# Kernel tuning notes

Hardware: AMD Instinct MI355X
Metric: run time of the kernel (lower is better)

The kernel has to match this reference:

```python
import jax, jax.numpy as jnp
import numpy as np

N_NODES = 100000
N_EDGES = 1600000
N_GRAPHS = 64
IN_DIM = 128
HID = 64
N_CLASSES = 10


def setup_inputs() -> dict:
    key = jax.random.key(0)
    ks = jax.random.split(key, 8)
    x = jax.random.normal(ks[0], (N_NODES, IN_DIM), jnp.float32)
    edge_index = jax.random.randint(ks[1], (2, N_EDGES), 0, N_NODES, jnp.int32)
    graph_id = jnp.sort(jax.random.randint(ks[2], (N_NODES,), 0, N_GRAPHS, jnp.int32))
    W1 = jax.random.normal(ks[3], (IN_DIM, HID), jnp.float32) / np.sqrt(IN_DIM)
    b1 = jnp.zeros((HID,), jnp.float32)
    W2 = jax.random.normal(ks[4], (HID, HID), jnp.float32) / np.sqrt(HID)
    b2 = jnp.zeros((HID,), jnp.float32)
    attn_W = jax.random.normal(ks[5], (HID, 1), jnp.float32) / np.sqrt(HID)
    attn_b = jnp.zeros((1,), jnp.float32)
    cls_W = jax.random.normal(ks[6], (HID, N_CLASSES), jnp.float32) / np.sqrt(HID)
    cls_b = jnp.zeros((N_CLASSES,), jnp.float32)
    return {"x": x, "edge_index": edge_index, "graph_id": graph_id,
            "W1": W1, "b1": b1, "W2": W2, "b2": b2,
            "attn_W": attn_W, "attn_b": attn_b, "cls_W": cls_W, "cls_b": cls_b}


def _graph_conv(h, W, b, src, dst, norm_out, norm_in):
    # DGL GraphConv, norm='both': D_in^{-1/2} A D_out^{-1/2} (h W) + b
    h = h @ W                                  # [N, out]
    h = h * norm_out[:, None]                  # scale by src out-degree^{-1/2}
    m = jax.ops.segment_sum(h[src], dst, num_segments=N_NODES)  # SpMM aggregation
    return m * norm_in[:, None] + b


def reference(x, edge_index, graph_id, W1, b1, W2, b2, attn_W, attn_b, cls_W, cls_b):
    src, dst = edge_index[0], edge_index[1]
    ones_e = jnp.ones((src.shape[0],), jnp.float32)
    deg_out = jnp.clip(jax.ops.segment_sum(ones_e, src, num_segments=N_NODES), 1.0)
    deg_in = jnp.clip(jax.ops.segment_sum(ones_e, dst, num_segments=N_NODES), 1.0)
    norm_out = jax.lax.rsqrt(deg_out)
    norm_in = jax.lax.rsqrt(deg_in)

    h = jax.nn.relu(_graph_conv(x, W1, b1, src, dst, norm_out, norm_in))
    h = jax.nn.relu(_graph_conv(h, W2, b2, src, dst, norm_out, norm_in))

    hw = jax.nn.sigmoid(h @ attn_W + attn_b)   # [N, 1] attention gate
    h = h * hw

    # mean_nodes: per-graph mean pooling
    sums = jax.ops.segment_sum(h, graph_id, num_segments=N_GRAPHS)        # [G, HID]
    cnts = jnp.clip(jax.ops.segment_sum(jnp.ones((N_NODES,), jnp.float32), graph_id,
                                        num_segments=N_GRAPHS), 1.0)
    hg = sums / cnts[:, None]
    out = hg @ cls_W + cls_b                   # [G, n_classes]
    return out, hw
```

## Files before the change

kernel.cpp:

```cpp
#include <hip/hip_runtime.h>
#include <stdint.h>


#define N_NODES   100000
#define N_EDGES   1600000
#define N_GRAPHS  64
#define IN_DIM    128
#define HID       64
#define N_CLASSES 10

#define NBUCK     391
#define P1B       196
#define EPB       8192
#define GB_BLOCKS 391
#define MTILES    6250
#define GEMM_BLOCKS 1563
#define SPMM_BLOCKS 3125
#define POOL_SLICES 32
#define WS_NEED   33885952u

typedef __attribute__((ext_vector_type(8))) short short8v;
typedef __attribute__((ext_vector_type(4))) float f32x4;
typedef __bf16 bf16x8 __attribute__((ext_vector_type(8)));

__device__ __forceinline__ f32x4 mfma16(short8v a, short8v b, f32x4 c) {
  return __builtin_amdgcn_mfma_f32_16x16x32_bf16(
      __builtin_bit_cast(bf16x8, a), __builtin_bit_cast(bf16x8, b), c, 0, 0, 0);
}

__device__ __forceinline__ float bf2f(unsigned short u) {
  unsigned int v = ((unsigned int)u) << 16;
  float f;
  __builtin_memcpy(&f, &v, 4);
  return f;
}

__device__ __forceinline__ unsigned short f2bf(float f) {
  unsigned int x;
  __builtin_memcpy(&x, &f, 4);
  unsigned int lsb = (x >> 16) & 1u;
  x += 0x7fffu + lsb;
  return (unsigned short)(x >> 16);
}

__device__ __forceinline__ void unpack_bf2(unsigned int u, float& lo, float& hi) {
  unsigned int a = u << 16;
  unsigned int b = u & 0xffff0000u;
  __builtin_memcpy(&lo, &a, 4);
  __builtin_memcpy(&hi, &b, 4);
}

__device__ __forceinline__ float ldf(const void* p, int i, int mode) {
  return mode ? bf2f(((const unsigned short*)p)[i]) : ((const float*)p)[i];
}

__global__ __launch_bounds__(256) void fallback_kernel(unsigned short* __restrict__ out,
                                                       int n) {
  int i = blockIdx.x * 256 + threadIdx.x;
  if (i < n) out[i] = 0;
}

__global__ __launch_bounds__(256) void wcvt_kernel(
    const unsigned short* __restrict__ xu,
    const void* __restrict__ W1, const void* __restrict__ W2,
    const void* __restrict__ b1, const void* __restrict__ b2,
    const void* __restrict__ attnW, const void* __restrict__ attnb,
    const void* __restrict__ clsW, const void* __restrict__ clsb,
    unsigned short* __restrict__ W1hf, unsigned short* __restrict__ W1lf,
    unsigned short* __restrict__ W2hf, unsigned short* __restrict__ W2lf,
    float* __restrict__ b1f, float* __restrict__ b2f,
    float* __restrict__ attnWf, float* __restrict__ attnbf,
    float* __restrict__ clsWf, float* __restrict__ clsbf,
    int* __restrict__ flag) {
  __shared__ int cnt[4];
  __shared__ int smode;
  int tid = (int)threadIdx.x;
  unsigned u = xu[2 * tid];
  int e = (int)((u >> 7) & 0xFF);
  int ok = (e >= 110 && e <= 132) ? 1 : 0;
  unsigned long long m = __ballot(ok);
  if ((tid & 63) == 0) cnt[tid >> 6] = __popcll(m);
  __syncthreads();
  if (tid == 0) {
    smode = (cnt[0] + cnt[1] + cnt[2] + cnt[3] > 128) ? 1 : 0;
    if (blockIdx.x == 0) {
      flag[0] = smode;
      flag[1] = 1;
    }
  }
  __syncthreads();
  int mode = smode;

  int i = blockIdx.x * 256 + tid;
  if (i < 1024) {
    int tile = i >> 6, lane = i & 63;
    int kt = tile >> 2, ct = tile & 3;
#pragma unroll
    for (int j = 0; j < 8; ++j) {
      int k = kt * 32 + ((lane >> 4) << 3) + j;
      int d = (ct << 4) + (lane & 15);
      float v = ldf(W1, k * HID + d, mode);
      unsigned short h = f2bf(v);
      unsigned short l = f2bf(v - bf2f(h));
      W1hf[i * 8 + j] = h;
      W1lf[i * 8 + j] = l;
    }
  } else if (i < 1536) {
    int ii = i - 1024;
    int tile = ii >> 6, lane = ii & 63;
    int kt = tile >> 2, ct = tile & 3;
#pragma unroll
    for (int j = 0; j < 8; ++j) {
      int k = kt * 32 + ((lane >> 4) << 3) + j;
      int d = (ct << 4) + (lane & 15);
      float v = ldf(W2, k * HID + d, mode);
      unsigned short h = f2bf(v);
      unsigned short l = f2bf(v - bf2f(h));
      W2hf[ii * 8 + j] = h;
      W2lf[ii * 8 + j] = l;
    }
  }
  if (i < HID) {
    b1f[i] = ldf(b1, i, mode);
    b2f[i] = ldf(b2, i, mode);
    attnWf[i] = ldf(attnW, i, mode);
  }
  if (i == 0) attnbf[0] = ldf(attnb, 0, mode);
  if (i < HID * N_CLASSES) clsWf[i] = ldf(clsW, i, mode);
  if (i < N_CLASSES) clsbf[i] = ldf(clsb, i, mode);
}

template <int K, bool SCALE>
__device__ __forceinline__ void gemm_tile(
    const void* __restrict__ A, const unsigned short* __restrict__ Whf,
    const unsigned short* __restrict__ Wlf, const float* __restrict__ norm_out,
    unsigned short* __restrict__ out, int mode, int mtile, int lane) {
  int n0 = mtile << 4;
  int row = lane & 15;
  int kg = lane >> 4;
  f32x4 acc0 = {0.f, 0.f, 0.f, 0.f};
  f32x4 acc1 = {0.f, 0.f, 0.f, 0.f};
  f32x4 acc2 = {0.f, 0.f, 0.f, 0.f};
  f32x4 acc3 = {0.f, 0.f, 0.f, 0.f};
  const short8v* whb0 = (const short8v*)Whf + lane;
  const short8v* wlb0 = (const short8v*)Wlf + lane;
  if (mode) {
    const unsigned short* xr = (const unsigned short*)A + (size_t)(n0 + row) * K + (kg << 3);
#pragma unroll
    for (int kt = 0; kt < K / 32; ++kt) {
      uint4 va = *(const uint4*)(xr + kt * 32);
      short8v xh = __builtin_bit_cast(short8v, va);
      const short8v* wh = whb0 + (size_t)(kt * 4) * 64;
      const short8v* wl = wlb0 + (size_t)(kt * 4) * 64;
      acc0 = mfma16(xh, wh[0], acc0);
      acc1 = mfma16(xh, wh[64], acc1);
      acc2 = mfma16(xh, wh[128], acc2);
      acc3 = mfma16(xh, wh[192], acc3);
      acc0 = mfma16(xh, wl[0], acc0);
      acc1 = mfma16(xh, wl[64], acc1);
      acc2 = mfma16(xh, wl[128], acc2);
      acc3 = mfma16(xh, wl[192], acc3);
    }
  } else {
    const float* xr = (const float*)A + (size_t)(n0 + row) * K + (kg << 3);
#pragma unroll
    for (int kt = 0; kt < K / 32; ++kt) {
      float4 a0 = *(const float4*)(xr + kt * 32);
      float4 a1 = *(const float4*)(xr + kt * 32 + 4);
      float xv[8] = {a0.x, a0.y, a0.z, a0.w, a1.x, a1.y, a1.z, a1.w};
      short8v xh, xl;
#pragma unroll
      for (int j = 0; j < 8; ++j) {
        unsigned short h = f2bf(xv[j]);
        unsigned short l = f2bf(xv[j] - bf2f(h));
        xh[j] = (short)h;
        xl[j] = (short)l;
      }
      const short8v* wh = whb0 + (size_t)(kt * 4) * 64;
      const short8v* wl = wlb0 + (size_t)(kt * 4) * 64;
      acc0 = mfma16(xh, wh[0], acc0);
      acc1 = mfma16(xh, wh[64], acc1);
      acc2 = mfma16(xh, wh[128], acc2);
      acc3 = mfma16(xh, wh[192], acc3);
      acc0 = mfma16(xh, wl[0], acc0);
      acc1 = mfma16(xh, wl[64], acc1);
      acc2 = mfma16(xh, wl[128], acc2);
      acc3 = mfma16(xh, wl[192], acc3);
      acc0 = mfma16(xl, wh[0], acc0);
      acc1 = mfma16(xl, wh[64], acc1);
      acc2 = mfma16(xl, wh[128], acc2);
      acc3 = mfma16(xl, wh[192], acc3);
    }
  }
  int col = lane & 15;
#pragma unroll
  for (int i = 0; i < 4; ++i) {
    int n = n0 + (kg << 2) + i;
    float s = SCALE ? norm_out[n] : 1.f;
    size_t rb = (size_t)n << 6;
    out[rb + col]      = f2bf(acc0[i] * s);
    out[rb + 16 + col] = f2bf(acc1[i] * s);
    out[rb + 32 + col] = f2bf(acc2[i] * s);
    out[rb + 48 + col] = f2bf(acc3[i] * s);
  }
}

__global__ __launch_bounds__(256) void fatA_kernel(
    const int* __restrict__ ei, int* __restrict__ blkhistD,
    int* __restrict__ blkhistS,
    const int* __restrict__ gid, int* __restrict__ gstart,
    const void* __restrict__ x, const unsigned short* __restrict__ W1hf,
    const unsigned short* __restrict__ W1lf, unsigned short* __restrict__ bufA,
    const int* __restrict__ flag) {
  int b = (int)blockIdx.x;
  int t = (int)threadIdx.x;
  if (b < P1B) {
    __shared__ int hD[NBUCK];
    __shared__ int hS[NBUCK];
    for (int i = t; i < NBUCK; i += 256) { hD[i] = 0; hS[i] = 0; }
    __syncthreads();
    int base_e = b * EPB;
    for (int s = 0; s < EPB / 1024; ++s) {
      int e4 = base_e + s * 1024 + t * 4;
      if (e4 < N_EDGES) {
        int4 s4 = *(const int4*)(ei + e4);
        int4 d4 = *(const int4*)(ei + N_EDGES + e4);
        int ss[4] = {s4.x, s4.y, s4.z, s4.w};
        int dd[4] = {d4.x, d4.y, d4.z, d4.w};
#pragma unroll
        for (int j = 0; j < 4; ++j) {
          if ((unsigned)ss[j] < N_NODES) atomicAdd(&hS[ss[j] >> 8], 1);
          if ((unsigned)dd[j] < N_NODES) atomicAdd(&hD[dd[j] >> 8], 1);
        }
      }
    }
    __syncthreads();
    for (int i = t; i < NBUCK; i += 256) {
      blkhistD[b * NBUCK + i] = hD[i];
      blkhistS[b * NBUCK + i] = hS[i];
    }
  } else if (b < P1B + GEMM_BLOCKS) {
    int mode = flag[0];
    int mtile = (b - P1B) * 4 + (t >> 6);
    if (mtile < MTILES)
      gemm_tile<IN_DIM, false>(x, W1hf, W1lf, (const float*)0, bufA, mode,
                               mtile, t & 63);
  } else {
    int bb = b - P1B - GEMM_BLOCKS;
    int n = bb * 256 + t;
    if (n >= N_NODES) return;
    int gc = gid[n] & (N_GRAPHS - 1);
    if (n == 0) {
      for (int g = 0; g <= gc; ++g) gstart[g] = 0;
    } else {
      int gp = gid[n - 1] & (N_GRAPHS - 1);
      for (int g = gp + 1; g <= gc; ++g) gstart[g] = n;
    }
    if (n == N_NODES - 1) {
      for (int g = gc + 1; g <= N_GRAPHS; ++g) gstart[g] = N_NODES;
    }
  }
}

__global__ __launch_bounds__(512) void bucket_scan_kernel(
    int* __restrict__ blkhistD, int* __restrict__ blkhistS,
    int* __restrict__ bstart_d, int* __restrict__ bstart_s) {
  int* hist = (blockIdx.x == 0) ? blkhistD : blkhistS;
  int* bst  = (blockIdx.x == 0) ? bstart_d : bstart_s;
  int u = (int)threadIdx.x;
  int tot = 0;
  if (u < NBUCK) {
    for (int blk = 0; blk < P1B; ++blk) tot += hist[blk * NBUCK + u];
  }
  __shared__ int smA[512];
  __shared__ int smB[512];
  smA[u] = tot;
  __syncthreads();
  int* a = smA;
  int* bq = smB;
  for (int off = 1; off < 512; off <<= 1) {
    int v = a[u];
    if (u >= off) v += a[u - off];
    bq[u] = v;
    __syncthreads();
    int* tmp = a; a = bq; bq = tmp;
  }
  int excl = a[u] - tot;
  if (u <= NBUCK) bst[u] = excl;
  if (u < NBUCK) {
    int off2 = excl;
    for (int blk = 0; blk < P1B; ++blk) {
      int h = hist[blk * NBUCK + u];
      hist[blk * NBUCK + u] = off2;
      off2 += h;
    }
  }
}

__global__ __launch_bounds__(256) void part_scatter_kernel(
    const int* __restrict__ ei, const int* __restrict__ blkbaseD,
    const int* __restrict__ blkbaseS,
    unsigned int* __restrict__ edstP, int* __restrict__ esrc) {
  __shared__ int cD[NBUCK];
  __shared__ int cS[NBUCK];
  int b = (int)blockIdx.x;
  int t = (int)threadIdx.x;
  for (int i = t; i < NBUCK; i += 256) {
    cD[i] = blkbaseD[b * NBUCK + i];
    cS[i] = blkbaseS[b * NBUCK + i];
  }
  __syncthreads();
  int base_e = b * EPB;
  for (int s = 0; s < EPB / 1024; ++s) {
    int e4 = base_e + s * 1024 + t * 4;
    if (e4 < N_EDGES) {
      int4 s4 = *(const int4*)(ei + e4);
      int4 d4 = *(const int4*)(ei + N_EDGES + e4);
      int ss[4] = {s4.x, s4.y, s4.z, s4.w};
      int dd[4] = {d4.x, d4.y, d4.z, d4.w};
#pragma unroll
      for (int j = 0; j < 4; ++j) {
        if ((unsigned)ss[j] < N_NODES) {
          int slot = atomicAdd(&cS[ss[j] >> 8], 1);
          esrc[slot] = ss[j];
        }
        if ((unsigned)dd[j] < N_NODES) {
          int slot = atomicAdd(&cD[dd[j] >> 8], 1);
          edstP[slot] = ((unsigned int)ss[j] << 8) | ((unsigned int)dd[j] & 255u);
        }
      }
    }
  }
}

__global__ __launch_bounds__(256) void csr_kernel(
    const unsigned int* __restrict__ edstP, const int* __restrict__ esrc,
    const int* __restrict__ bstart_d, const int* __restrict__ bstart_s,
    int* __restrict__ rowptr, int* __restrict__ colx,
    float* __restrict__ norm_in, float* __restrict__ norm_out) {
  __shared__ int lc[256];
  __shared__ int smA[256];
  __shared__ int smB[256];
  int b = (int)blockIdx.x;
  int t = (int)threadIdx.x;
  if (b < NBUCK) {
    int node0 = b << 8;
    int base = bstart_d[b];
    int end  = bstart_d[b + 1];
    lc[t] = 0;
    __syncthreads();
    for (int i = base + t; i < end; i += 256) {
      unsigned int p = edstP[i];
      atomicAdd(&lc[p & 255u], 1);
    }
    __syncthreads();
    int my = lc[t];
    smA[t] = my;
    __syncthreads();
    int* a = smA;
    int* bq = smB;
    for (int off = 1; off < 256; off <<= 1) {
      int v = a[t];
      if (t >= off) v += a[t - off];
      bq[t] = v;
      __syncthreads();
      int* tmp = a; a = bq; bq = tmp;
    }
    int excl = a[t] - my;
    int n = node0 + t;
    if (n <= N_NODES) rowptr[n] = base + excl;
    if (n < N_NODES) {
      int c = my < 1 ? 1 : my;
      norm_in[n] = rsqrtf((float)c);
    }
    __syncthreads();
    lc[t] = base + excl;
    __syncthreads();
    for (int i = base + t; i < end; i += 256) {
      unsigned int p = edstP[i];
      int slot = atomicAdd(&lc[p & 255u], 1);
      colx[slot] = (int)(p >> 8);
    }
  } else {
    int bb = b - NBUCK;
    int node0 = bb << 8;
    int base = bstart_s[bb];
    int end  = bstart_s[bb + 1];
    lc[t] = 0;
    __syncthreads();
    for (int i = base + t; i < end; i += 256) {
      atomicAdd(&lc[esrc[i] - node0], 1);
    }
    __syncthreads();
    int n = node0 + t;
    if (n < N_NODES) {
      int c = lc[t] < 1 ? 1 : lc[t];
      norm_out[n] = rsqrtf((float)c);
    }
  }
}

template <int K>
__global__ __launch_bounds__(256) void gemm_mfma_kernel(
    const void* __restrict__ A, const unsigned short* __restrict__ Whf,
    const unsigned short* __restrict__ Wlf, const float* __restrict__ norm_out,
    unsigned short* __restrict__ out, const int* __restrict__ flag) {
  int mode = flag[0];
  int mtile = (int)blockIdx.x * 4 + ((int)threadIdx.x >> 6);
  if (mtile >= MTILES) return;
  gemm_tile<K, true>(A, Whf, Wlf, norm_out, out, mode, mtile,
                     (int)threadIdx.x & 63);
}

__device__ __forceinline__ void accum8f(uint4 v, float no, float acc[8]) {
  float lo, hi;
  unpack_bf2(v.x, lo, hi); acc[0] = fmaf(lo, no, acc[0]); acc[1] = fmaf(hi, no, acc[1]);
  unpack_bf2(v.y, lo, hi); acc[2] = fmaf(lo, no, acc[2]); acc[3] = fmaf(hi, no, acc[3]);
  unpack_bf2(v.z, lo, hi); acc[4] = fmaf(lo, no, acc[4]); acc[5] = fmaf(hi, no, acc[5]);
  unpack_bf2(v.w, lo, hi); acc[6] = fmaf(lo, no, acc[6]); acc[7] = fmaf(hi, no, acc[7]);
}

__device__ __forceinline__ void spmm_gather8s(const unsigned short* __restrict__ hs,
                                              const int* __restrict__ col,
                                              const float* __restrict__ no,
                                              int e0, int e1, int dim0,
                                              float acc[8]) {
  int e = e0;
  for (; e + 4 <= e1; e += 4) {
    unsigned c0 = (unsigned)col[e];
    unsigned c1 = (unsigned)col[e + 1];
    unsigned c2 = (unsigned)col[e + 2];
    unsigned c3 = (unsigned)col[e + 3];
    uint4 v0 = make_uint4(0u, 0u, 0u, 0u);
    uint4 v1 = v0, v2 = v0, v3 = v0;
    float n0 = 0.f, n1 = 0.f, n2 = 0.f, n3 = 0.f;
    if (c0 < N_NODES) { v0 = *(const uint4*)(hs + ((size_t)c0 << 6) + dim0); n0 = no[c0]; }
    if (c1 < N_NODES) { v1 = *(const uint4*)(hs + ((size_t)c1 << 6) + dim0); n1 = no[c1]; }
    if (c2 < N_NODES) { v2 = *(const uint4*)(hs + ((size_t)c2 << 6) + dim0); n2 = no[c2]; }
    if (c3 < N_NODES) { v3 = *(const uint4*)(hs + ((size_t)c3 << 6) + dim0); n3 = no[c3]; }
    accum8f(v0, n0, acc);
    accum8f(v1, n1, acc);
    accum8f(v2, n2, acc);
    accum8f(v3, n3, acc);
  }
  for (; e < e1; ++e) {
    unsigned c = (unsigned)col[e];
    uint4 v = make_uint4(0u, 0u, 0u, 0u);
    float nn = 0.f;
    if (c < N_NODES) { v = *(const uint4*)(hs + ((size_t)c << 6) + dim0); nn = no[c]; }
    accum8f(v, nn, acc);
  }
}

__device__ __forceinline__ void accum8(uint4 v, float acc[8]) {
  float lo, hi;
  unpack_bf2(v.x, lo, hi); acc[0] += lo; acc[1] += hi;
  unpack_bf2(v.y, lo, hi); acc[2] += lo; acc[3] += hi;
  unpack_bf2(v.z, lo, hi); acc[4] += lo; acc[5] += hi;
  unpack_bf2(v.w, lo, hi); acc[6] += lo; acc[7] += hi;
}

__device__ __forceinline__ void spmm_gather8(const unsigned short* __restrict__ hs,
                                             const int* __restrict__ col,
                                             int e0, int e1, int dim0,
                                             float acc[8]) {
  int e = e0;
  for (; e + 4 <= e1; e += 4) {
    unsigned c0 = (unsigned)col[e];
    unsigned c1 = (unsigned)col[e + 1];
    unsigned c2 = (unsigned)col[e + 2];
    unsigned c3 = (unsigned)col[e + 3];
    uint4 v0 = make_uint4(0u, 0u, 0u, 0u);
    uint4 v1 = v0, v2 = v0, v3 = v0;
    if (c0 < N_NODES) v0 = *(const uint4*)(hs + ((size_t)c0 << 6) + dim0);
    if (c1 < N_NODES) v1 = *(const uint4*)(hs + ((size_t)c1 << 6) + dim0);
    if (c2 < N_NODES) v2 = *(const uint4*)(hs + ((size_t)c2 << 6) + dim0);
    if (c3 < N_NODES) v3 = *(const uint4*)(hs + ((size_t)c3 << 6) + dim0);
    accum8(v0, acc);
    accum8(v1, acc);
    accum8(v2, acc);
    accum8(v3, acc);
  }
  for (; e < e1; ++e) {
    unsigned c = (unsigned)col[e];
    uint4 v = make_uint4(0u, 0u, 0u, 0u);
    if (c < N_NODES) v = *(const uint4*)(hs + ((size_t)c << 6) + dim0);
    accum8(v, acc);
  }
}

__global__ __launch_bounds__(256) void spmm_kernel(const unsigned short* __restrict__ hs,
                                                   const int* __restrict__ rowptr,
                                                   const int* __restrict__ col,
                                                   const float* __restrict__ norm_out,
                                                   const float* __restrict__ norm_in,
                                                   const float* __restrict__ b1f,
                                                   unsigned short* __restrict__ out) {
  int n = (int)(blockIdx.x * 32 + (threadIdx.x >> 3));
  int dim0 = ((int)threadIdx.x & 7) << 3;
  if (n >= N_NODES) return;
  int e0 = rowptr[n], e1 = rowptr[n + 1];
  if (e0 < 0) e0 = 0;
  if (e1 > N_EDGES) e1 = N_EDGES;
  float acc[8];
#pragma unroll
  for (int i = 0; i < 8; ++i) acc[i] = 0.f;
  spmm_gather8s(hs, col, norm_out, e0, e1, dim0, acc);
  float nin = norm_in[n];
  unsigned int pk[4];
#pragma unroll
  for (int i = 0; i < 4; ++i) {
    float vlo = fmaxf(acc[2 * i] * nin + b1f[dim0 + 2 * i], 0.f);
    float vhi = fmaxf(acc[2 * i + 1] * nin + b1f[dim0 + 2 * i + 1], 0.f);
    pk[i] = (unsigned int)f2bf(vlo) | ((unsigned int)f2bf(vhi) << 16);
  }
  *(uint4*)(out + ((size_t)n << 6) + dim0) = make_uint4(pk[0], pk[1], pk[2], pk[3]);
}

__global__ __launch_bounds__(256) void spmm_attn_kernel(
    const unsigned short* __restrict__ hs,
    const int* __restrict__ rowptr, const int* __restrict__ col,
    const float* __restrict__ norm_in, const float* __restrict__ b2f,
    const float* __restrict__ attnWf, const float* __restrict__ attnbf,
    void* __restrict__ out_base, unsigned short* __restrict__ gated,
    const int* __restrict__ flag) {
  int mode = flag[0];
  int n = (int)(blockIdx.x * 32 + (threadIdx.x >> 3));
  int dim0 = ((int)threadIdx.x & 7) << 3;
  if (n >= N_NODES) return;
  int e0 = rowptr[n], e1 = rowptr[n + 1];
  if (e0 < 0) e0 = 0;
  if (e1 > N_EDGES) e1 = N_EDGES;
  float acc[8];
#pragma unroll
  for (int i = 0; i < 8; ++i) acc[i] = 0.f;
  spmm_gather8(hs, col, e0, e1, dim0, acc);
  float nin = norm_in[n];
  float vv[8];
  float p = 0.f;
#pragma unroll
  for (int i = 0; i < 8; ++i) {
    vv[i] = fmaxf(acc[i] * nin + b2f[dim0 + i], 0.f);
    p += vv[i] * attnWf[dim0 + i];
  }
#pragma unroll
  for (int m = 1; m <= 4; m <<= 1) p += __shfl_xor(p, m, 64);
  float logit = p + attnbf[0];
  float hwv = 1.f / (1.f + __expf(-logit));
  if ((threadIdx.x & 7) == 0) {
    if (mode) ((unsigned short*)out_base)[N_GRAPHS * N_CLASSES + n] = f2bf(hwv);
    else      ((float*)out_base)[N_GRAPHS * N_CLASSES + n] = hwv;
  }
  unsigned int pk[4];
#pragma unroll
  for (int i = 0; i < 4; ++i) {
    pk[i] = (unsigned int)f2bf(vv[2 * i] * hwv) |
            ((unsigned int)f2bf(vv[2 * i + 1] * hwv) << 16);
  }
  *(uint4*)(gated + ((size_t)n << 6) + dim0) = make_uint4(pk[0], pk[1], pk[2], pk[3]);
}

__global__ __launch_bounds__(256) void pool_kernel(const unsigned short* __restrict__ gated,
                                                   const int* __restrict__ gstart,
                                                   float* __restrict__ gpart) {
  int g = (int)blockIdx.x >> 5;
  int s = (int)blockIdx.x & 31;
  int dim = (int)threadIdx.x & 63;
  int rsel = (int)threadIdx.x >> 6;
  int r0 = gstart[g], r1 = gstart[g + 1];
  if (r0 < 0) r0 = 0;
  if (r1 > N_NODES) r1 = N_NODES;
  int len = r1 - r0;
  if (len < 0) len = 0;
  int a = r0 + (int)(((long long)len * s) >> 5);
  int bnd = r0 + (int)(((long long)len * (s + 1)) >> 5);
  float acc = 0.f;
  for (int r = a + rsel; r < bnd; r += 4)
    acc += bf2f(gated[((size_t)r << 6) + dim]);
  __shared__ float sm[256];
  sm[threadIdx.x] = acc;
  __syncthreads();
  if (threadIdx.x < 64)
    gpart[((size_t)blockIdx.x << 6) + dim] =
        sm[dim] + sm[64 + dim] + sm[128 + dim] + sm[192 + dim];
}

__global__ __launch_bounds__(640) void final_kernel(const float* __restrict__ gpart,
                                                    const int* __restrict__ gstart,
                                                    const float* __restrict__ clsWf,
                                                    const float* __restrict__ clsbf,
                                                    void* __restrict__ out_base,
                                                    const int* __restrict__ flag) {
  __shared__ float gs[N_GRAPHS * HID];
  int t = (int)threadIdx.x;
  for (int idx = t; idx < N_GRAPHS * HID; idx += 640) {
    int g = idx >> 6, d = idx & 63;
    float a = 0.f;
#pragma unroll
    for (int s = 0; s < POOL_SLICES; ++s)
      a += gpart[(((size_t)(g << 5) + s) << 6) + d];
    gs[idx] = a;
  }
  __syncthreads();
  int mode = flag[0];
  if (t >= N_GRAPHS * N_CLASSES) return;
  int g = t / N_CLASSES, c = t - g * N_CLASSES;
  int cg = gstart[g + 1] - gstart[g];
  if (cg < 1) cg = 1;
  float inv = 1.f / (float)cg;
  float acc = 0.f;
#pragma unroll
  for (int d = 0; d < HID; ++d) acc += gs[(g << 6) + d] * clsWf[d * N_CLASSES + c];
  float r = acc * inv + clsbf[c];
  if (mode) ((unsigned short*)out_base)[t] = f2bf(r);
  else      ((float*)out_base)[t] = r;
}

extern "C" void kernel_launch(void* const* d_in, const int* in_sizes, int n_in,
                              void* d_out, int out_size, void* d_ws, size_t ws_size,
                              hipStream_t stream) {
  const void* x     = d_in[0];
  const int*  ei    = (const int*)d_in[1];
  const int*  gid   = (const int*)d_in[2];
  const void* W1    = d_in[3];
  const void* b1    = d_in[4];
  const void* W2    = d_in[5];
  const void* b2    = d_in[6];
  const void* attnW = d_in[7];
  const void* attnb = d_in[8];
  const void* clsW  = d_in[9];
  const void* clsb  = d_in[10];

  if (ws_size < (size_t)WS_NEED) {
    fallback_kernel<<<(out_size + 255) / 256, 256, 0, stream>>>(
        (unsigned short*)d_out, out_size);
    return;
  }

  char* w = (char*)d_ws;
  int*   flag     = (int*)(w + 0);
  int*   gstart   = (int*)(w + 64);
  float* gsum_un  = (float*)(w + 576);
  int*   bstart_d = (int*)(w + 16960);
  int*   bstart_s = (int*)(w + 18560);
  int*   blkhD    = (int*)(w + 20160);
  int*   blkhS    = (int*)(w + 326720);
  int*   rowptr   = (int*)(w + 633280);
  float* norm_out = (float*)(w + 1033344);
  float* norm_in  = (float*)(w + 1433344);
  unsigned short* W1hf = (unsigned short*)(w + 1833344);
  unsigned short* W1lf = (unsigned short*)(w + 1849728);
  unsigned short* W2hf = (unsigned short*)(w + 1866112);
  unsigned short* W2lf = (unsigned short*)(w + 1874304);
  float* b1f      = (float*)(w + 1882496);
  float* b2f      = (float*)(w + 1882752);
  float* attnWf   = (float*)(w + 1883008);
  float* attnbf   = (float*)(w + 1883264);
  float* clsWf    = (float*)(w + 1883328);
  float* clsbf    = (float*)(w + 1885888);
  int*   colx     = (int*)(w + 1885952);
  unsigned int* edstP = (unsigned int*)(w + 8285952);
  int*   esrc     = (int*)(w + 14685952);
  unsigned short* bufA = (unsigned short*)(w + 21085952);
  unsigned short* bufB = (unsigned short*)(w + 8285952);
  float* gpart    = (float*)(w + 20160);
  (void)gsum_un;

  wcvt_kernel<<<32, 256, 0, stream>>>((const unsigned short*)x, W1, W2, b1, b2,
                                      attnW, attnb, clsW, clsb, W1hf, W1lf,
                                      W2hf, W2lf, b1f, b2f, attnWf, attnbf,
                                      clsWf, clsbf, flag);

  fatA_kernel<<<P1B + GEMM_BLOCKS + GB_BLOCKS, 256, 0, stream>>>(
      ei, blkhD, blkhS, gid, gstart, x, W1hf, W1lf, bufA, flag);

  bucket_scan_kernel<<<2, 512, 0, stream>>>(blkhD, blkhS, bstart_d, bstart_s);
  part_scatter_kernel<<<P1B, 256, 0, stream>>>(ei, blkhD, blkhS, edstP, esrc);
  csr_kernel<<<2 * NBUCK, 256, 0, stream>>>(edstP, esrc, bstart_d, bstart_s,
                                            rowptr, colx, norm_in, norm_out);

  spmm_kernel<<<SPMM_BLOCKS, 256, 0, stream>>>(bufA, rowptr, colx, norm_out,
                                               norm_in, b1f, bufB);

  gemm_mfma_kernel<HID><<<GEMM_BLOCKS, 256, 0, stream>>>(
      bufB, W2hf, W2lf, norm_out, bufA, flag + 1);
  spmm_attn_kernel<<<SPMM_BLOCKS, 256, 0, stream>>>(
      bufA, rowptr, colx, norm_in, b2f, attnWf, attnbf, d_out, bufB, flag);

  pool_kernel<<<N_GRAPHS * POOL_SLICES, 256, 0, stream>>>(bufB, gstart, gpart);
  final_kernel<<<1, 640, 0, stream>>>(gpart, gstart, clsWf, clsbf, d_out, flag);
}
```

Baseline: 270.0 us.

## Degree-sort nodes per bucket for SpMM and parallelize bucket base scan

The csr kernel now builds a per-256-node permutation that orders nodes by in-degree, and both SpMM kernels pick their node through this permutation. Neighbouring 8-lane groups in a wave then carry similar edge counts, which is meant to cut divergence and load imbalance in the gather loops. The block histogram layout is transposed and the serial per-bucket offset scan is moved into a new many-block kernel. Bounds checks on column indices in the gather loops are dropped, saving instructions but trusting the CSR to hold only valid indices.

```diff
diff --git a/kernel.cpp b/kernel.cpp
--- a/kernel.cpp
+++ b/kernel.cpp
@@ -15,7 +15,8 @@
 #define GB_BLOCKS 391
 #define MTILES    6250
 #define GEMM_BLOCKS 1563
-#define SPMM_BLOCKS 3125
+#define NSLOT     (NBUCK * 256)
+#define SPMM_BLOCKS 3128
 #define POOL_SLICES 32
 #define WS_NEED   33885952u
 
@@ -236,8 +237,8 @@
     }
     __syncthreads();
     for (int i = t; i < NBUCK; i += 256) {
-      blkhistD[b * NBUCK + i] = hD[i];
-      blkhistS[b * NBUCK + i] = hS[i];
+      blkhistD[i * P1B + b] = hD[i];
+      blkhistS[i * P1B + b] = hS[i];
     }
   } else if (b < P1B + GEMM_BLOCKS) {
     int mode = flag[0];
@@ -262,15 +263,16 @@
   }
 }
 
-__global__ __launch_bounds__(512) void bucket_scan_kernel(
-    int* __restrict__ blkhistD, int* __restrict__ blkhistS,
+__global__ __launch_bounds__(512) void bucket_tot_kernel(
+    const int* __restrict__ blkhistD, const int* __restrict__ blkhistS,
     int* __restrict__ bstart_d, int* __restrict__ bstart_s) {
-  int* hist = (blockIdx.x == 0) ? blkhistD : blkhistS;
+  const int* hist = (blockIdx.x == 0) ? blkhistD : blkhistS;
   int* bst  = (blockIdx.x == 0) ? bstart_d : bstart_s;
   int u = (int)threadIdx.x;
   int tot = 0;
   if (u < NBUCK) {
-    for (int blk = 0; blk < P1B; ++blk) tot += hist[blk * NBUCK + u];
+    const int* row = hist + u * P1B;
+    for (int blk = 0; blk < P1B; ++blk) tot += row[blk];
   }
   __shared__ int smA[512];
   __shared__ int smB[512];
@@ -287,14 +289,32 @@
   }
   int excl = a[u] - tot;
   if (u <= NBUCK) bst[u] = excl;
-  if (u < NBUCK) {
-    int off2 = excl;
-    for (int blk = 0; blk < P1B; ++blk) {
-      int h = hist[blk * NBUCK + u];
-      hist[blk * NBUCK + u] = off2;
-      off2 += h;
-    }
-  }
+}
+
+__global__ __launch_bounds__(256) void bucket_base_kernel(
+    int* __restrict__ blkhistD, int* __restrict__ blkhistS,
+    const int* __restrict__ bstart_d, const int* __restrict__ bstart_s) {
+  int bb = (int)blockIdx.x;
+  int* hist = (bb < NBUCK) ? blkhistD : blkhistS;
+  const int* bst = (bb < NBUCK) ? bstart_d : bstart_s;
+  int u = (bb < NBUCK) ? bb : bb - NBUCK;
+  int t = (int)threadIdx.x;
+  int h = (t < P1B) ? hist[u * P1B + t] : 0;
+  __shared__ int smA[256];
+  __shared__ int smB[256];
+  smA[t] = h;
+  __syncthreads();
+  int* a = smA;
+  int* bq = smB;
+  for (int off = 1; off < 256; off <<= 1) {
+    int v = a[t];
+    if (t >= off) v += a[t - off];
+    bq[t] = v;
+    __syncthreads();
+    int* tmp = a; a = bq; bq = tmp;
+  }
+  int excl = a[t] - h;
+  if (t < P1B) hist[u * P1B + t] = bst[u] + excl;
 }
 
 __global__ __launch_bounds__(256) void part_scatter_kernel(
@@ -306,8 +326,8 @@
   int b = (int)blockIdx.x;
   int t = (int)threadIdx.x;
   for (int i = t; i < NBUCK; i += 256) {
-    cD[i] = blkbaseD[b * NBUCK + i];
-    cS[i] = blkbaseS[b * NBUCK + i];
+    cD[i] = blkbaseD[i * P1B + b];
+    cS[i] = blkbaseS[i * P1B + b];
   }
   __syncthreads();
   int base_e = b * EPB;
@@ -337,7 +357,8 @@
     const unsigned int* __restrict__ edstP, const int* __restrict__ esrc,
     const int* __restrict__ bstart_d, const int* __restrict__ bstart_s,
     int* __restrict__ rowptr, int* __restrict__ colx,
-    float* __restrict__ norm_in, float* __restrict__ norm_out) {
+    float* __restrict__ norm_in, float* __restrict__ norm_out,
+    int* __restrict__ perm) {
   __shared__ int lc[256];
   __shared__ int smA[256];
   __shared__ int smB[256];
@@ -381,6 +402,30 @@
       int slot = atomicAdd(&lc[p & 255u], 1);
       colx[slot] = (int)(p >> 8);
     }
+    __syncthreads();
+    int deg = my < 255 ? my : 255;
+    lc[t] = 0;
+    __syncthreads();
+    atomicAdd(&lc[deg], 1);
+    __syncthreads();
+    int hv = lc[t];
+    smA[t] = hv;
+    __syncthreads();
+    int* a2 = smA;
+    int* b2 = smB;
+    for (int off = 1; off < 256; off <<= 1) {
+      int v = a2[t];
+      if (t >= off) v += a2[t - off];
+      b2[t] = v;
+      __syncthreads();
+      int* tmp = a2; a2 = b2; b2 = tmp;
+    }
+    int hexcl = a2[t] - hv;
+    __syncthreads();
+    lc[t] = hexcl;
+    __syncthreads();
+    int rank = atomicAdd(&lc[deg], 1);
+    perm[(b << 8) + rank] = n;
   } else {
     int bb = b - NBUCK;
     int node0 = bb << 8;
@@ -427,28 +472,21 @@
                                               float acc[8]) {
   int e = e0;
   for (; e + 4 <= e1; e += 4) {
-    unsigned c0 = (unsigned)col[e];
-    unsigned c1 = (unsigned)col[e + 1];
-    unsigned c2 = (unsigned)col[e + 2];
-    unsigned c3 = (unsigned)col[e + 3];
-    uint4 v0 = make_uint4(0u, 0u, 0u, 0u);
-    uint4 v1 = v0, v2 = v0, v3 = v0;
-    float n0 = 0.f, n1 = 0.f, n2 = 0.f, n3 = 0.f;
-    if (c0 < N_NODES) { v0 = *(const uint4*)(hs + ((size_t)c0 << 6) + dim0); n0 = no[c0]; }
-    if (c1 < N_NODES) { v1 = *(const uint4*)(hs + ((size_t)c1 << 6) + dim0); n1 = no[c1]; }
-    if (c2 < N_NODES) { v2 = *(const uint4*)(hs + ((size_t)c2 << 6) + dim0); n2 = no[c2]; }
-    if (c3 < N_NODES) { v3 = *(const uint4*)(hs + ((size_t)c3 << 6) + dim0); n3 = no[c3]; }
+    int c0 = col[e], c1 = col[e + 1], c2 = col[e + 2], c3 = col[e + 3];
+    float n0 = no[c0], n1 = no[c1], n2 = no[c2], n3 = no[c3];
+    uint4 v0 = *(const uint4*)(hs + ((size_t)c0 << 6) + dim0);
+    uint4 v1 = *(const uint4*)(hs + ((size_t)c1 << 6) + dim0);
+    uint4 v2 = *(const uint4*)(hs + ((size_t)c2 << 6) + dim0);
+    uint4 v3 = *(const uint4*)(hs + ((size_t)c3 << 6) + dim0);
     accum8f(v0, n0, acc);
     accum8f(v1, n1, acc);
     accum8f(v2, n2, acc);
     accum8f(v3, n3, acc);
   }
   for (; e < e1; ++e) {
-    unsigned c = (unsigned)col[e];
-    uint4 v = make_uint4(0u, 0u, 0u, 0u);
-    float nn = 0.f;
-    if (c < N_NODES) { v = *(const uint4*)(hs + ((size_t)c << 6) + dim0); nn = no[c]; }
-    accum8f(v, nn, acc);
+    int c = col[e];
+    uint4 v = *(const uint4*)(hs + ((size_t)c << 6) + dim0);
+    accum8f(v, no[c], acc);
   }
 }
 
@@ -466,25 +504,19 @@
                                              float acc[8]) {
   int e = e0;
   for (; e + 4 <= e1; e += 4) {
-    unsigned c0 = (unsigned)col[e];
-    unsigned c1 = (unsigned)col[e + 1];
-    unsigned c2 = (unsigned)col[e + 2];
-    unsigned c3 = (unsigned)col[e + 3];
-    uint4 v0 = make_uint4(0u, 0u, 0u, 0u);
-    uint4 v1 = v0, v2 = v0, v3 = v0;
-    if (c0 < N_NODES) v0 = *(const uint4*)(hs + ((size_t)c0 << 6) + dim0);
-    if (c1 < N_NODES) v1 = *(const uint4*)(hs + ((size_t)c1 << 6) + dim0);
-    if (c2 < N_NODES) v2 = *(const uint4*)(hs + ((size_t)c2 << 6) + dim0);
-    if (c3 < N_NODES) v3 = *(const uint4*)(hs + ((size_t)c3 << 6) + dim0);
+    int c0 = col[e], c1 = col[e + 1], c2 = col[e + 2], c3 = col[e + 3];
+    uint4 v0 = *(const uint4*)(hs + ((size_t)c0 << 6) + dim0);
+    uint4 v1 = *(const uint4*)(hs + ((size_t)c1 << 6) + dim0);
+    uint4 v2 = *(const uint4*)(hs + ((size_t)c2 << 6) + dim0);
+    uint4 v3 = *(const uint4*)(hs + ((size_t)c3 << 6) + dim0);
     accum8(v0, acc);
     accum8(v1, acc);
     accum8(v2, acc);
     accum8(v3, acc);
   }
   for (; e < e1; ++e) {
-    unsigned c = (unsigned)col[e];
-    uint4 v = make_uint4(0u, 0u, 0u, 0u);
-    if (c < N_NODES) v = *(const uint4*)(hs + ((size_t)c << 6) + dim0);
+    int c = col[e];
+    uint4 v = *(const uint4*)(hs + ((size_t)c << 6) + dim0);
     accum8(v, acc);
   }
 }
@@ -495,10 +527,12 @@
                                                    const float* __restrict__ norm_out,
                                                    const float* __restrict__ norm_in,
                                                    const float* __restrict__ b1f,
+                                                   const int* __restrict__ perm,
                                                    unsigned short* __restrict__ out) {
-  int n = (int)(blockIdx.x * 32 + (threadIdx.x >> 3));
+  int slot = (int)(blockIdx.x * 32 + (threadIdx.x >> 3));
+  int n = perm[slot];
+  if ((unsigned)n >= N_NODES) return;
   int dim0 = ((int)threadIdx.x & 7) << 3;
-  if (n >= N_NODES) return;
   int e0 = rowptr[n], e1 = rowptr[n + 1];
   if (e0 < 0) e0 = 0;
   if (e1 > N_EDGES) e1 = N_EDGES;
@@ -522,12 +556,14 @@
     const int* __restrict__ rowptr, const int* __restrict__ col,
     const float* __restrict__ norm_in, const float* __restrict__ b2f,
     const float* __restrict__ attnWf, const float* __restrict__ attnbf,
+    const int* __restrict__ perm,
     void* __restrict__ out_base, unsigned short* __restrict__ gated,
     const int* __restrict__ flag) {
   int mode = flag[0];
-  int n = (int)(blockIdx.x * 32 + (threadIdx.x >> 3));
+  int slot = (int)(blockIdx.x * 32 + (threadIdx.x >> 3));
+  int n = perm[slot];
+  if ((unsigned)n >= N_NODES) return;
   int dim0 = ((int)threadIdx.x & 7) << 3;
-  if (n >= N_NODES) return;
   int e0 = rowptr[n], e1 = rowptr[n + 1];
   if (e0 < 0) e0 = 0;
   if (e1 > N_EDGES) e1 = N_EDGES;
@@ -640,7 +676,6 @@
   char* w = (char*)d_ws;
   int*   flag     = (int*)(w + 0);
   int*   gstart   = (int*)(w + 64);
-  float* gsum_un  = (float*)(w + 576);
   int*   bstart_d = (int*)(w + 16960);
   int*   bstart_s = (int*)(w + 18560);
   int*   blkhD    = (int*)(w + 20160);
@@ -663,8 +698,8 @@
   int*   esrc     = (int*)(w + 14685952);
   unsigned short* bufA = (unsigned short*)(w + 21085952);
   unsigned short* bufB = (unsigned short*)(w + 8285952);
+  int*   perm     = (int*)(w + 20160);
   float* gpart    = (float*)(w + 20160);
-  (void)gsum_un;
 
   wcvt_kernel<<<32, 256, 0, stream>>>((const unsigned short*)x, W1, W2, b1, b2,
                                       attnW, attnb, clsW, clsb, W1hf, W1lf,
@@ -674,18 +709,20 @@
   fatA_kernel<<<P1B + GEMM_BLOCKS + GB_BLOCKS, 256, 0, stream>>>(
       ei, blkhD, blkhS, gid, gstart, x, W1hf, W1lf, bufA, flag);
 
-  bucket_scan_kernel<<<2, 512, 0, stream>>>(blkhD, blkhS, bstart_d, bstart_s);
+  bucket_tot_kernel<<<2, 512, 0, stream>>>(blkhD, blkhS, bstart_d, bstart_s);
+  bucket_base_kernel<<<2 * NBUCK, 256, 0, stream>>>(blkhD, blkhS, bstart_d, bstart_s);
+
   part_scatter_kernel<<<P1B, 256, 0, stream>>>(ei, blkhD, blkhS, edstP, esrc);
   csr_kernel<<<2 * NBUCK, 256, 0, stream>>>(edstP, esrc, bstart_d, bstart_s,
-                                            rowptr, colx, norm_in, norm_out);
+                                            rowptr, colx, norm_in, norm_out, perm);
 
   spmm_kernel<<<SPMM_BLOCKS, 256, 0, stream>>>(bufA, rowptr, colx, norm_out,
-                                               norm_in, b1f, bufB);
+                                               norm_in, b1f, perm, bufB);
 
   gemm_mfma_kernel<HID><<<GEMM_BLOCKS, 256, 0, stream>>>(
       bufB, W2hf, W2lf, norm_out, bufA, flag + 1);
   spmm_attn_kernel<<<SPMM_BLOCKS, 256, 0, stream>>>(
-      bufA, rowptr, colx, norm_in, b2f, attnWf, attnbf, d_out, bufB, flag);
+      bufA, rowptr, colx, norm_in, b2f, attnWf, attnbf, perm, d_out, bufB, flag);
 
   pool_kernel<<<N_GRAPHS * POOL_SLICES, 256, 0, stream>>>(bufB, gstart, gpart);
   final_kernel<<<1, 640, 0, stream>>>(gpart, gstart, clsWf, clsbf, d_out, flag);
```

New measurement: 287.7 us. 6.5% more time.
